# Kernel tuning notes

Measured on AMD Instinct MI355X. Metric: run time of the kernel, lower is better.

## Reference

```python
import jax, jax.numpy as jnp
import numpy as np

N_NODES = 1_000_000
N_EDGES = 16_000_000
RATIO = 0.5


def setup_inputs() -> dict:
    key = jax.random.key(0)
    k1, k2, k3 = jax.random.split(key, 3)
    x = jax.random.normal(k1, (N_NODES, 3), dtype=jnp.float32)
    edge_index = jax.random.randint(k2, (2, N_EDGES), 0, N_NODES, dtype=jnp.int32)
    weight = jax.random.normal(k3, (3,), dtype=jnp.float32)
    return {"x": x, "edge_index": edge_index, "weight": weight}


def reference(x, edge_index, weight):
    # PyG TopKPooling with in_channels=3, ratio=0.5, nonlinearity=tanh, min_score=None
    n = x.shape[0]
    k = int(np.ceil(RATIO * n))
    # per-node score: tanh( (x . w) / ||w|| )
    score = jnp.tanh((x @ weight) / jnp.linalg.norm(weight))  # [N]
    top_scores, perm = jax.lax.top_k(score, k)                # [k], [k]
    # gate selected node features by their score
    x_out = x[perm] * top_scores[:, None]                     # [k, 3]
    # relabel nodes: old index -> new index (or -1 if dropped)
    new_idx = jnp.full((n,), -1, dtype=edge_index.dtype)
    new_idx = new_idx.at[perm].set(jnp.arange(k, dtype=edge_index.dtype))
    new_edges = new_idx[edge_index]                           # [2, E]
    edge_mask = (new_edges[0] >= 0) & (new_edges[1] >= 0)     # [E]
    # jit-friendly fixed-shape output: invalid edges marked -1 + boolean mask
    new_edges = jnp.where(edge_mask[None, :], new_edges, -1)
    return x_out, new_edges, edge_mask
```

## Files before the change

kernel.cpp:

```cpp
#include <hip/hip_runtime.h>


#define N_NODES 1000000
#define N_EDGES 16000000
#define K_SEL   500000

typedef int      v4i __attribute__((ext_vector_type(4)));
typedef float    v4f __attribute__((ext_vector_type(4)));
typedef unsigned v4u __attribute__((ext_vector_type(4)));
typedef unsigned long long u64;

static constexpr int NDIG     = 256;
static constexpr int STHREADS = 256;
static constexpr int SIPT     = 8;
static constexpr int SCHUNK   = STHREADS * SIPT;
static constexpr int NB       = (N_NODES + SCHUNK - 1) / SCHUNK;
static constexpr int NWAVE    = STHREADS / 64;

static constexpr int EB_THREADS = 1024;
static constexpr int EB_EDGES   = EB_THREADS * 8;
static constexpr int NODE_SPLIT = 524288;
static constexpr int BM_WORDS   = (N_NODES + 31) / 32;
static constexpr int BM_W0      = NODE_SPLIT / 32;
static constexpr int BM_W1      = BM_WORDS - BM_W0;
static constexpr int BM_ALLOC   = 31264;

__device__ __forceinline__ float tanh_xla(float x) {
  const float kCutoff = 0.0004f;
  const float kClamp  = 7.90531110763549805f;
  float ax = fabsf(x);
  float xc = fminf(fmaxf(x, -kClamp), kClamp);
  float x2 = __fmul_rn(xc, xc);
  float p = -2.76076847742355e-16f;
  p = __fadd_rn(__fmul_rn(p, x2),  2.00018790482477e-13f);
  p = __fadd_rn(__fmul_rn(p, x2), -8.60467152213735e-11f);
  p = __fadd_rn(__fmul_rn(p, x2),  5.12229709037114e-08f);
  p = __fadd_rn(__fmul_rn(p, x2),  1.48572235717979e-05f);
  p = __fadd_rn(__fmul_rn(p, x2),  6.37261928875436e-04f);
  p = __fadd_rn(__fmul_rn(p, x2),  4.89352455891786e-03f);
  float num = __fmul_rn(xc, p);
  float q = 1.19825839466702e-06f;
  q = __fadd_rn(__fmul_rn(q, x2), 1.18534705686654e-04f);
  q = __fadd_rn(__fmul_rn(q, x2), 2.26843463243900e-03f);
  q = __fadd_rn(__fmul_rn(q, x2), 4.89352518554385e-03f);
  float r = __fdiv_rn(num, q);
  return (ax < kCutoff) ? x : r;
}

__global__ void score_kernel(const float* __restrict__ x, const float* __restrict__ w,
                             float* __restrict__ score, u64* __restrict__ kp, int n) {
  int i = blockIdx.x * blockDim.x + threadIdx.x;
  if (i >= n) return;
  float w0 = w[0], w1 = w[1], w2 = w[2];
  float nrm = __fsqrt_rn(__fadd_rn(__fadd_rn(__fmul_rn(w0, w0), __fmul_rn(w1, w1)),
                                   __fmul_rn(w2, w2)));
  float dot = __fadd_rn(__fadd_rn(__fmul_rn(x[3*i+0], w0), __fmul_rn(x[3*i+1], w1)),
                        __fmul_rn(x[3*i+2], w2));
  float z = __fdiv_rn(dot, nrm);
  float s = tanh_xla(z);
  score[i] = s;
  unsigned u = __float_as_uint(s);
  if (u == 0x80000000u) u = 0u;
  u = (u & 0x80000000u) ? ~u : (u | 0x80000000u);
  kp[i] = ((u64)(~u) << 32) | (unsigned)i;
}

__global__ void radix_hist(const u64* __restrict__ kp, int n,
                           unsigned* __restrict__ histDM, int shift) {
  __shared__ unsigned h[NDIG];
  int t = threadIdx.x;
  h[t] = 0;
  __syncthreads();
  int base = blockIdx.x * SCHUNK;
#pragma unroll
  for (int it = 0; it < SCHUNK / 256; ++it) {
    int i = base + it * 256 + t;
    if (i < n) atomicAdd(&h[(unsigned)(kp[i] >> (32 + shift)) & 255u], 1u);
  }
  __syncthreads();
  histDM[t * NB + blockIdx.x] = h[t];
}

__global__ void scan_rows(unsigned* __restrict__ histDM, unsigned* __restrict__ rowsum) {
  __shared__ unsigned lds[512];
  int d = blockIdx.x, t = threadIdx.x;
  unsigned v = (t < NB) ? histDM[d * NB + t] : 0u;
  lds[t] = v;
  __syncthreads();
#pragma unroll
  for (int off = 1; off < 512; off <<= 1) {
    unsigned add = (t >= off) ? lds[t - off] : 0u;
    __syncthreads();
    lds[t] += add;
    __syncthreads();
  }
  if (t < NB) histDM[d * NB + t] = lds[t] - v;
  if (t == 511) rowsum[d] = lds[511];
}

__global__ __launch_bounds__(STHREADS) void radix_scatter(
    const u64* __restrict__ kpin, int n,
    const unsigned* __restrict__ histDM, const unsigned* __restrict__ rowsum,
    u64* __restrict__ kpout, int shift) {
  __shared__ unsigned short whist[SIPT][NWAVE][NDIG];
  __shared__ unsigned goff[NDIG];
  __shared__ unsigned bexcl[NDIG];
  __shared__ unsigned scanbuf[NDIG];
  __shared__ u64 lkp[SCHUNK];
  int t = threadIdx.x, b = blockIdx.x;
  int wave = t >> 6, lane = t & 63;
  for (int j = t; j < SIPT * NWAVE * NDIG; j += STHREADS)
    ((unsigned short*)whist)[j] = 0;
  unsigned rs = rowsum[t];
  scanbuf[t] = rs;
  __syncthreads();
#pragma unroll
  for (int o = 1; o < NDIG; o <<= 1) {
    unsigned add = (t >= o) ? scanbuf[t - o] : 0u;
    __syncthreads();
    scanbuf[t] += add;
    __syncthreads();
  }
  goff[t] = (scanbuf[t] - rs) + histDM[t * NB + b];
  __syncthreads();

  u64 k[SIPT];
  unsigned dg[SIPT], lr[SIPT];
  bool val[SIPT];
  int base = b * SCHUNK;
#pragma unroll
  for (int s = 0; s < SIPT; ++s) {
    int i = base + s * STHREADS + t;
    val[s] = (i < n);
    k[s] = val[s] ? kpin[i] : 0ull;
    dg[s] = (unsigned)(k[s] >> (32 + shift)) & 255u;
  }
#pragma unroll
  for (int s = 0; s < SIPT; ++s) {
    unsigned long long m = ~0ull;
#pragma unroll
    for (int bb = 0; bb < 8; ++bb) {
      unsigned long long vote = __ballot((dg[s] >> bb) & 1u);
      m &= ((dg[s] >> bb) & 1u) ? vote : ~vote;
    }
    m &= __ballot(val[s]);
    lr[s] = (unsigned)__popcll(m & ((1ull << lane) - 1ull));
    if (val[s] && lr[s] == 0)
      whist[s][wave][dg[s]] = (unsigned short)__popcll(m);
  }
  __syncthreads();
  unsigned run = 0;
#pragma unroll
  for (int s = 0; s < SIPT; ++s)
#pragma unroll
    for (int w = 0; w < NWAVE; ++w) {
      unsigned c = whist[s][w][t];
      whist[s][w][t] = (unsigned short)run;
      run += c;
    }
  scanbuf[t] = run;
  __syncthreads();
#pragma unroll
  for (int o = 1; o < NDIG; o <<= 1) {
    unsigned add = (t >= o) ? scanbuf[t - o] : 0u;
    __syncthreads();
    scanbuf[t] += add;
    __syncthreads();
  }
  bexcl[t] = scanbuf[t] - run;
  __syncthreads();
#pragma unroll
  for (int s = 0; s < SIPT; ++s) {
    if (val[s]) {
      unsigned lp = bexcl[dg[s]] + (unsigned)whist[s][wave][dg[s]] + lr[s];
      lkp[lp] = k[s];
    }
  }
  __syncthreads();
  int nvalid = min(n - base, SCHUNK);
#pragma unroll
  for (int s = 0; s < SIPT; ++s) {
    int j = s * STHREADS + t;
    if (j < nvalid) {
      u64 kk = lkp[j];
      unsigned d = (unsigned)(kk >> (32 + shift)) & 255u;
      unsigned gpos = goff[d] + ((unsigned)j - bexcl[d]);
      kpout[gpos] = kk;
    }
  }
}

__global__ void init_kernel(int* __restrict__ ni, unsigned* __restrict__ bm, int n) {
  int i = blockIdx.x * blockDim.x + threadIdx.x;
  if (i < n) ni[i] = -1;
  if (i < BM_ALLOC) bm[i] = 0u;
}

__global__ void select_kernel(const u64* __restrict__ kp, const float* __restrict__ score,
                              const float* __restrict__ x, int* __restrict__ ni,
                              unsigned* __restrict__ bm, float* __restrict__ xout, int k) {
  int i = blockIdx.x * blockDim.x + threadIdx.x;
  if (i >= k) return;
  int pidx = (int)(unsigned)(kp[i] & 0xFFFFFFFFull);
  ni[pidx] = i;
  atomicOr(&bm[pidx >> 5], 1u << (pidx & 31));
  float s = score[pidx];
  xout[3*i+0] = __fmul_rn(x[3*pidx+0], s);
  xout[3*i+1] = __fmul_rn(x[3*pidx+1], s);
  xout[3*i+2] = __fmul_rn(x[3*pidx+2], s);
}

__global__ __launch_bounds__(EB_THREADS) void edge_kernel(
    const int* __restrict__ ei, const int* __restrict__ ni,
    const unsigned* __restrict__ bm,
    float* __restrict__ oedge, float* __restrict__ omask) {
  __shared__ unsigned lbm[BM_W0];
  int t = threadIdx.x;
  long long e = (long long)blockIdx.x * EB_EDGES + (long long)t * 8;
  bool act = (e + 8 <= (long long)N_EDGES);

  v4i a0{}, a1{}, b0{}, b1{};
  if (act) {
    a0 = __builtin_nontemporal_load((const v4i*)(ei + e));
    a1 = __builtin_nontemporal_load((const v4i*)(ei + e) + 1);
    b0 = __builtin_nontemporal_load((const v4i*)(ei + (long long)N_EDGES + e));
    b1 = __builtin_nontemporal_load((const v4i*)(ei + (long long)N_EDGES + e) + 1);
  }
  int A[8], B[8];
#pragma unroll
  for (int j = 0; j < 4; ++j) {
    A[j] = a0[j]; A[4 + j] = a1[j];
    B[j] = b0[j]; B[4 + j] = b1[j];
  }

#pragma unroll
  for (int j = 0; j < BM_W0 / (EB_THREADS * 4); ++j)
    ((v4u*)lbm)[t + j * EB_THREADS] = ((const v4u*)bm)[t + j * EB_THREADS];
  __syncthreads();
  unsigned bA = 0, bB = 0;
  if (act) {
#pragma unroll
    for (int j = 0; j < 8; ++j) {
      if (A[j] < NODE_SPLIT) bA |= ((lbm[A[j] >> 5] >> (A[j] & 31)) & 1u) << j;
      if (B[j] < NODE_SPLIT) bB |= ((lbm[B[j] >> 5] >> (B[j] & 31)) & 1u) << j;
    }
  }
  __syncthreads();
  {
    const v4u* src = (const v4u*)(bm + BM_W0);
    for (int j = t; j < (BM_W1 + 3) / 4; j += EB_THREADS)
      ((v4u*)lbm)[j] = src[j];
  }
  __syncthreads();
  if (act) {
#pragma unroll
    for (int j = 0; j < 8; ++j) {
      if (A[j] >= NODE_SPLIT) {
        int q = A[j] - NODE_SPLIT;
        bA |= ((lbm[q >> 5] >> (q & 31)) & 1u) << j;
      }
      if (B[j] >= NODE_SPLIT) {
        int q = B[j] - NODE_SPLIT;
        bB |= ((lbm[q >> 5] >> (q & 31)) & 1u) << j;
      }
    }
    unsigned mm = bA & bB;
    float fa[8], fb[8], fm[8];
#pragma unroll
    for (int j = 0; j < 8; ++j) {
      bool m = (mm >> j) & 1u;
      int na = -1, nb = -1;
      if (m) { na = ni[A[j]]; nb = ni[B[j]]; }
      fa[j] = m ? (float)na : -1.0f;
      fb[j] = m ? (float)nb : -1.0f;
      fm[j] = m ? 1.0f : 0.0f;
    }
    __builtin_nontemporal_store(*(const v4f*)&fa[0], (v4f*)(oedge + e));
    __builtin_nontemporal_store(*(const v4f*)&fa[4], (v4f*)(oedge + e) + 1);
    __builtin_nontemporal_store(*(const v4f*)&fb[0], (v4f*)(oedge + (long long)N_EDGES + e));
    __builtin_nontemporal_store(*(const v4f*)&fb[4], (v4f*)(oedge + (long long)N_EDGES + e) + 1);
    __builtin_nontemporal_store(*(const v4f*)&fm[0], (v4f*)(omask + e));
    __builtin_nontemporal_store(*(const v4f*)&fm[4], (v4f*)(omask + e) + 1);
  }
}

extern "C" void kernel_launch(void* const* d_in, const int* in_sizes, int n_in,
                              void* d_out, int out_size, void* d_ws, size_t ws_size,
                              hipStream_t stream) {
  const float* x  = (const float*)d_in[0];
  const int*   ei = (const int*)d_in[1];
  const float* w  = (const float*)d_in[2];
  float* out = (float*)d_out;

  char* ws = (char*)d_ws;
  size_t off = 0;
  auto alloc = [&](size_t bytes) -> void* {
    void* ptr = ws + off;
    off += (bytes + 255) & ~size_t(255);
    return ptr;
  };
  float*    score  = (float*)alloc((size_t)N_NODES * 4);
  u64*      kp0    = (u64*)alloc((size_t)N_NODES * 8);
  u64*      kp1    = (u64*)alloc((size_t)N_NODES * 8);
  unsigned* histDM = (unsigned*)alloc((size_t)NDIG * NB * 4);
  unsigned* rowsum = (unsigned*)alloc((size_t)NDIG * 4);
  int*      ni     = (int*)alloc((size_t)N_NODES * 4);
  unsigned* bm     = (unsigned*)alloc((size_t)BM_ALLOC * 4);
  (void)ws_size; (void)in_sizes; (void)n_in; (void)out_size;

  score_kernel<<<(N_NODES + 255) / 256, 256, 0, stream>>>(x, w, score, kp0, N_NODES);

  u64* kb[2] = {kp0, kp1};
  int cur = 0;
  for (int pass = 0; pass < 4; ++pass) {
    int shift = pass * 8;
    radix_hist   <<<NB,   256, 0, stream>>>(kb[cur], N_NODES, histDM, shift);
    scan_rows    <<<NDIG, 512, 0, stream>>>(histDM, rowsum);
    radix_scatter<<<NB, STHREADS, 0, stream>>>(kb[cur], N_NODES, histDM, rowsum,
                                               kb[cur ^ 1], shift);
    cur ^= 1;
  }
  init_kernel  <<<(N_NODES + 255) / 256, 256, 0, stream>>>(ni, bm, N_NODES);
  select_kernel<<<(K_SEL + 255) / 256, 256, 0, stream>>>(kb[cur], score, x, ni, bm, out, K_SEL);
  edge_kernel  <<<(N_EDGES + EB_EDGES - 1) / EB_EDGES, EB_THREADS, 0, stream>>>(
      ei, ni, bm, out + 1500000, out + 33500000);
}
```

Measured before the change: 230.1 us.

## Fuse score and radix top-k into one cooperative kernel; use whole-bitmap LDS edge kernel

Replaces the chain of about fourteen launches (score, four rounds of hist/scan/scatter, init, select) with one cooperative kernel that uses grid.sync between phases. It also folds the next pass's histogram into the tail of each scatter, and runs node init and selection inside that kernel. The edge kernel becomes a persistent 256-block grid that loads the full node bitmap (about 125KB) into dynamic LDS once per block, instead of two half-bitmap loads per block. Risks: the cooperative launch needs all NB (489) blocks of 256 threads with large LDS to be co-resident, otherwise it falls back to the old chain. The big-LDS edge kernel may limit occupancy to one block per CU.

Result: slower. 898.8 us (+290.7%).

```diff
diff --git a/kernel.cpp b/kernel.cpp
--- a/kernel.cpp
+++ b/kernel.cpp
@@ -1,4 +1,7 @@
 #include <hip/hip_runtime.h>
+#include <hip/hip_cooperative_groups.h>
+
+namespace cg = cooperative_groups;
 
 
 #define N_NODES 1000000
@@ -19,6 +22,7 @@
 
 static constexpr int EB_THREADS = 1024;
 static constexpr int EB_EDGES   = EB_THREADS * 8;
+static constexpr int NCHUNK     = (N_EDGES + EB_EDGES - 1) / EB_EDGES;
 static constexpr int NODE_SPLIT = 524288;
 static constexpr int BM_WORDS   = (N_NODES + 31) / 32;
 static constexpr int BM_W0      = NODE_SPLIT / 32;
@@ -47,6 +51,187 @@
   return (ax < kCutoff) ? x : r;
 }
 
+__global__ __launch_bounds__(STHREADS) void topk_coop(
+    const float* __restrict__ x, const float* __restrict__ w,
+    float* __restrict__ score, u64* __restrict__ kp0, u64* __restrict__ kp1,
+    unsigned* __restrict__ histDM, unsigned* __restrict__ rowsum,
+    int* __restrict__ ni, unsigned* __restrict__ bm, float* __restrict__ xout) {
+  cg::grid_group grid = cg::this_grid();
+  __shared__ unsigned short whist[SIPT][NWAVE][NDIG];
+  __shared__ unsigned goff[NDIG];
+  __shared__ unsigned bexcl[NDIG];
+  __shared__ unsigned scanbuf[NDIG];
+  __shared__ u64 lkp[SCHUNK];
+  const int t = threadIdx.x, b = blockIdx.x;
+  const int wave = t >> 6, lane = t & 63;
+  const int base = b * SCHUNK;
+
+  goff[t] = 0;
+  __syncthreads();
+  {
+    float w0 = w[0], w1 = w[1], w2 = w[2];
+    float nrm = __fsqrt_rn(__fadd_rn(__fadd_rn(__fmul_rn(w0, w0), __fmul_rn(w1, w1)),
+                                     __fmul_rn(w2, w2)));
+#pragma unroll
+    for (int s = 0; s < SIPT; ++s) {
+      int i = base + s * STHREADS + t;
+      if (i < N_NODES) {
+        ni[i] = -1;
+        float dot = __fadd_rn(__fadd_rn(__fmul_rn(x[3*i+0], w0), __fmul_rn(x[3*i+1], w1)),
+                              __fmul_rn(x[3*i+2], w2));
+        float z = __fdiv_rn(dot, nrm);
+        float sc = tanh_xla(z);
+        score[i] = sc;
+        unsigned u = __float_as_uint(sc);
+        if (u == 0x80000000u) u = 0u;
+        u = (u & 0x80000000u) ? ~u : (u | 0x80000000u);
+        unsigned key = ~u;
+        kp0[i] = ((u64)key << 32) | (unsigned)i;
+        atomicAdd(&goff[key & 255u], 1u);
+      }
+    }
+    if (t < 64) { int wi = b * 64 + t; if (wi < BM_ALLOC) bm[wi] = 0u; }
+  }
+  __syncthreads();
+  histDM[t * NB + b] = goff[t];
+  grid.sync();
+
+  for (int pass = 0; pass < 4; ++pass) {
+    const u64* kin = (pass & 1) ? kp1 : kp0;
+    u64* kout      = (pass & 1) ? kp0 : kp1;
+    const int sh = 32 + 8 * pass;
+
+    if (b < NDIG) {
+      unsigned v0 = (2*t     < NB) ? histDM[b*NB + 2*t]     : 0u;
+      unsigned v1 = (2*t + 1 < NB) ? histDM[b*NB + 2*t + 1] : 0u;
+      unsigned ps = v0 + v1;
+      scanbuf[t] = ps;
+      __syncthreads();
+#pragma unroll
+      for (int o = 1; o < NDIG; o <<= 1) {
+        unsigned add = (t >= o) ? scanbuf[t - o] : 0u;
+        __syncthreads();
+        scanbuf[t] += add;
+        __syncthreads();
+      }
+      unsigned excl = scanbuf[t] - ps;
+      if (2*t     < NB) histDM[b*NB + 2*t]     = excl;
+      if (2*t + 1 < NB) histDM[b*NB + 2*t + 1] = excl + v0;
+      if (t == NDIG - 1) rowsum[b] = scanbuf[t];
+    }
+    grid.sync();
+
+    {
+      for (int j = t; j < SIPT * NWAVE * NDIG; j += STHREADS)
+        ((unsigned short*)whist)[j] = 0;
+      unsigned rs = rowsum[t];
+      scanbuf[t] = rs;
+      __syncthreads();
+#pragma unroll
+      for (int o = 1; o < NDIG; o <<= 1) {
+        unsigned add = (t >= o) ? scanbuf[t - o] : 0u;
+        __syncthreads();
+        scanbuf[t] += add;
+        __syncthreads();
+      }
+      goff[t] = (scanbuf[t] - rs) + histDM[t * NB + b];
+      __syncthreads();
+
+      u64 k[SIPT];
+      unsigned dg[SIPT], lr[SIPT];
+      bool val[SIPT];
+#pragma unroll
+      for (int s = 0; s < SIPT; ++s) {
+        int i = base + s * STHREADS + t;
+        val[s] = (i < N_NODES);
+        k[s] = val[s] ? kin[i] : 0ull;
+        dg[s] = (unsigned)(k[s] >> sh) & 255u;
+      }
+#pragma unroll
+      for (int s = 0; s < SIPT; ++s) {
+        unsigned long long m = ~0ull;
+#pragma unroll
+        for (int bb = 0; bb < 8; ++bb) {
+          unsigned long long vote = __ballot((dg[s] >> bb) & 1u);
+          m &= ((dg[s] >> bb) & 1u) ? vote : ~vote;
+        }
+        m &= __ballot(val[s]);
+        lr[s] = (unsigned)__popcll(m & ((1ull << lane) - 1ull));
+        if (val[s] && lr[s] == 0)
+          whist[s][wave][dg[s]] = (unsigned short)__popcll(m);
+      }
+      __syncthreads();
+      unsigned run = 0;
+#pragma unroll
+      for (int s = 0; s < SIPT; ++s)
+#pragma unroll
+        for (int wv = 0; wv < NWAVE; ++wv) {
+          unsigned c = whist[s][wv][t];
+          whist[s][wv][t] = (unsigned short)run;
+          run += c;
+        }
+      scanbuf[t] = run;
+      __syncthreads();
+#pragma unroll
+      for (int o = 1; o < NDIG; o <<= 1) {
+        unsigned add = (t >= o) ? scanbuf[t - o] : 0u;
+        __syncthreads();
+        scanbuf[t] += add;
+        __syncthreads();
+      }
+      bexcl[t] = scanbuf[t] - run;
+      __syncthreads();
+#pragma unroll
+      for (int s = 0; s < SIPT; ++s)
+        if (val[s]) {
+          unsigned lp = bexcl[dg[s]] + (unsigned)whist[s][wave][dg[s]] + lr[s];
+          lkp[lp] = k[s];
+        }
+      __syncthreads();
+      int nvalid = min(N_NODES - base, SCHUNK);
+#pragma unroll
+      for (int s = 0; s < SIPT; ++s) {
+        int j = s * STHREADS + t;
+        if (j < nvalid) {
+          u64 kk = lkp[j];
+          unsigned d = (unsigned)(kk >> sh) & 255u;
+          kout[goff[d] + ((unsigned)j - bexcl[d])] = kk;
+        }
+      }
+    }
+    grid.sync();
+
+    if (pass < 3) {
+      goff[t] = 0;
+      __syncthreads();
+      const int sh2 = sh + 8;
+#pragma unroll
+      for (int s = 0; s < SIPT; ++s) {
+        int i = base + s * STHREADS + t;
+        if (i < N_NODES) atomicAdd(&goff[(unsigned)(kout[i] >> sh2) & 255u], 1u);
+      }
+      __syncthreads();
+      histDM[t * NB + b] = goff[t];
+      grid.sync();
+    }
+  }
+
+#pragma unroll
+  for (int s = 0; s < 4; ++s) {
+    int i = b * 1024 + s * STHREADS + t;
+    if (i < K_SEL) {
+      u64 kk = kp0[i];
+      int pidx = (int)(unsigned)(kk & 0xFFFFFFFFull);
+      ni[pidx] = i;
+      atomicOr(&bm[pidx >> 5], 1u << (pidx & 31));
+      float sc = score[pidx];
+      xout[3*i+0] = __fmul_rn(x[3*pidx+0], sc);
+      xout[3*i+1] = __fmul_rn(x[3*pidx+1], sc);
+      xout[3*i+2] = __fmul_rn(x[3*pidx+2], sc);
+    }
+  }
+}
+
 __global__ void score_kernel(const float* __restrict__ x, const float* __restrict__ w,
                              float* __restrict__ score, u64* __restrict__ kp, int n) {
   int i = blockIdx.x * blockDim.x + threadIdx.x;
@@ -184,8 +369,7 @@
     if (j < nvalid) {
       u64 kk = lkp[j];
       unsigned d = (unsigned)(kk >> (32 + shift)) & 255u;
-      unsigned gpos = goff[d] + ((unsigned)j - bexcl[d]);
-      kpout[gpos] = kk;
+      kpout[goff[d] + ((unsigned)j - bexcl[d])] = kk;
     }
   }
 }
@@ -210,6 +394,53 @@
   xout[3*i+2] = __fmul_rn(x[3*pidx+2], s);
 }
 
+__global__ __launch_bounds__(EB_THREADS) void edge_big(
+    const int* __restrict__ ei, const int* __restrict__ ni,
+    const unsigned* __restrict__ bm,
+    float* __restrict__ oedge, float* __restrict__ omask) {
+  extern __shared__ unsigned lbm[];
+  for (int j = threadIdx.x; j < BM_ALLOC / 4; j += EB_THREADS)
+    ((v4u*)lbm)[j] = ((const v4u*)bm)[j];
+  __syncthreads();
+  for (int c = blockIdx.x; c < NCHUNK; c += gridDim.x) {
+    long long e = (long long)c * EB_EDGES + (long long)threadIdx.x * 8;
+    if (e + 8 > (long long)N_EDGES) continue;
+    v4i a0 = __builtin_nontemporal_load((const v4i*)(ei + e));
+    v4i a1 = __builtin_nontemporal_load((const v4i*)(ei + e) + 1);
+    v4i b0 = __builtin_nontemporal_load((const v4i*)(ei + (long long)N_EDGES + e));
+    v4i b1 = __builtin_nontemporal_load((const v4i*)(ei + (long long)N_EDGES + e) + 1);
+    int A[8], B[8];
+#pragma unroll
+    for (int j = 0; j < 4; ++j) {
+      A[j] = a0[j]; A[4 + j] = a1[j];
+      B[j] = b0[j]; B[4 + j] = b1[j];
+    }
+    unsigned mA = 0, mB = 0;
+#pragma unroll
+    for (int j = 0; j < 8; ++j) {
+      mA |= ((lbm[A[j] >> 5] >> (A[j] & 31)) & 1u) << j;
+      mB |= ((lbm[B[j] >> 5] >> (B[j] & 31)) & 1u) << j;
+    }
+    unsigned mm = mA & mB;
+    float fa[8], fb[8], fm[8];
+#pragma unroll
+    for (int j = 0; j < 8; ++j) {
+      bool m = (mm >> j) & 1u;
+      int na = -1, nb = -1;
+      if (m) { na = ni[A[j]]; nb = ni[B[j]]; }
+      fa[j] = m ? (float)na : -1.0f;
+      fb[j] = m ? (float)nb : -1.0f;
+      fm[j] = m ? 1.0f : 0.0f;
+    }
+    __builtin_nontemporal_store(*(const v4f*)&fa[0], (v4f*)(oedge + e));
+    __builtin_nontemporal_store(*(const v4f*)&fa[4], (v4f*)(oedge + e) + 1);
+    __builtin_nontemporal_store(*(const v4f*)&fb[0], (v4f*)(oedge + (long long)N_EDGES + e));
+    __builtin_nontemporal_store(*(const v4f*)&fb[4], (v4f*)(oedge + (long long)N_EDGES + e) + 1);
+    __builtin_nontemporal_store(*(const v4f*)&fm[0], (v4f*)(omask + e));
+    __builtin_nontemporal_store(*(const v4f*)&fm[4], (v4f*)(omask + e) + 1);
+  }
+}
+
 __global__ __launch_bounds__(EB_THREADS) void edge_kernel(
     const int* __restrict__ ei, const int* __restrict__ ni,
     const unsigned* __restrict__ bm,
@@ -232,7 +463,6 @@
     A[j] = a0[j]; A[4 + j] = a1[j];
     B[j] = b0[j]; B[4 + j] = b1[j];
   }
-
 #pragma unroll
   for (int j = 0; j < BM_W0 / (EB_THREADS * 4); ++j)
     ((v4u*)lbm)[t + j * EB_THREADS] = ((const v4u*)bm)[t + j * EB_THREADS];
@@ -308,20 +538,43 @@
   unsigned* bm     = (unsigned*)alloc((size_t)BM_ALLOC * 4);
   (void)ws_size; (void)in_sizes; (void)n_in; (void)out_size;
 
-  score_kernel<<<(N_NODES + 255) / 256, 256, 0, stream>>>(x, w, score, kp0, N_NODES);
-
-  u64* kb[2] = {kp0, kp1};
-  int cur = 0;
-  for (int pass = 0; pass < 4; ++pass) {
-    int shift = pass * 8;
-    radix_hist   <<<NB,   256, 0, stream>>>(kb[cur], N_NODES, histDM, shift);
-    scan_rows    <<<NDIG, 512, 0, stream>>>(histDM, rowsum);
-    radix_scatter<<<NB, STHREADS, 0, stream>>>(kb[cur], N_NODES, histDM, rowsum,
-                                               kb[cur ^ 1], shift);
-    cur ^= 1;
-  }
-  init_kernel  <<<(N_NODES + 255) / 256, 256, 0, stream>>>(ni, bm, N_NODES);
-  select_kernel<<<(K_SEL + 255) / 256, 256, 0, stream>>>(kb[cur], score, x, ni, bm, out, K_SEL);
-  edge_kernel  <<<(N_EDGES + EB_EDGES - 1) / EB_EDGES, EB_THREADS, 0, stream>>>(
-      ei, ni, bm, out + 1500000, out + 33500000);
-}
+  void* kargs[] = {(void*)&x, (void*)&w, (void*)&score, (void*)&kp0, (void*)&kp1,
+                   (void*)&histDM, (void*)&rowsum, (void*)&ni, (void*)&bm, (void*)&out};
+  hipError_t ce = hipLaunchCooperativeKernel((const void*)topk_coop, dim3(NB),
+                                             dim3(STHREADS), kargs, 0, stream);
+  if (ce != hipSuccess) {
+    score_kernel<<<(N_NODES + 255) / 256, 256, 0, stream>>>(x, w, score, kp0, N_NODES);
+    u64* kb[2] = {kp0, kp1};
+    int cur = 0;
+    for (int pass = 0; pass < 4; ++pass) {
+      int shift = pass * 8;
+      radix_hist   <<<NB,   256, 0, stream>>>(kb[cur], N_NODES, histDM, shift);
+      scan_rows    <<<NDIG, 512, 0, stream>>>(histDM, rowsum);
+      radix_scatter<<<NB, STHREADS, 0, stream>>>(kb[cur], N_NODES, histDM, rowsum,
+                                                 kb[cur ^ 1], shift);
+      cur ^= 1;
+    }
+    init_kernel  <<<(N_NODES + 255) / 256, 256, 0, stream>>>(ni, bm, N_NODES);
+    select_kernel<<<(K_SEL + 255) / 256, 256, 0, stream>>>(kb[cur], score, x, ni, bm, out, K_SEL);
+  }
+
+  int dev = 0;
+  hipGetDevice(&dev);
+  int maxShm = 0;
+  hipDeviceGetAttribute(&maxShm, hipDeviceAttributeMaxSharedMemoryPerMultiprocessor, dev);
+  size_t need = (size_t)BM_ALLOC * 4;
+  bool big = false;
+  if ((size_t)maxShm >= need) {
+    if (hipFuncSetAttribute((const void*)edge_big,
+                            hipFuncAttributeMaxDynamicSharedMemorySize,
+                            (int)need) == hipSuccess)
+      big = true;
+  }
+  if (big) {
+    edge_big<<<256, EB_THREADS, need, stream>>>(ei, ni, bm,
+                                                out + 1500000, out + 33500000);
+  } else {
+    edge_kernel<<<(N_EDGES + EB_EDGES - 1) / EB_EDGES, EB_THREADS, 0, stream>>>(
+        ei, ni, bm, out + 1500000, out + 33500000);
+  }
+}
```
